# Kernel optimization log

Measured on AMD Instinct MI355X. Metric: run time of the kernel, lower is better.

## Reference

```python
import jax, jax.numpy as jnp
import numpy as np

Nx, Nu, Ny, Np, H = 2, 1, 2, 8, 32
Nz = Np * (Nx + Nu)  # 24
B, T = 4096, 256
F, V, Delta = 0.1, 1.0, 1.0  # ps.squeeze(), volume, sample time
ymean = jnp.array([0.5, 0.5], jnp.float32)
ystd = jnp.array([0.3, 0.2], jnp.float32)
umean = jnp.array([1.0], jnp.float32)
ustd = jnp.array([0.5], jnp.float32)


def fnn(x, params):
    # dense layers: tanh hidden, linear output
    for W, b in params[:-1]:
        x = jnp.tanh(x @ W + b)
    W, b = params[-1]
    return x @ W + b


def fxzu(x, z, u, p1, p2, p3):
    # dCa/dt = F*(Caf-Ca)/V - r1 ; dCb/dt = -F*Cb/V + r1 - 3*r2 + r3
    Castd, Cbstd = ystd[0:1], ystd[1:2]
    r1 = fnn(x[:, 0:1], p1) * Castd
    r2 = fnn(x[:, 1:2], p2) * Cbstd
    r3 = fnn(z, p3) * Cbstd
    xs = x * ystd + ymean
    us = u * ustd + umean
    Ca, Cb, Caf = xs[:, 0:1], xs[:, 1:2], us[:, 0:1]
    dCa = F * (Caf - Ca) / V - r1
    dCb = -F * Cb / V + r1 - 3.0 * r2 + r3
    return jnp.concatenate([dCa, dCb], axis=-1) / ystd


def interp(yseq):
    # (B,(Np+1)*Nx) -> (B, Np*Nx): midpoints of consecutive Nx-blocks
    b = yseq.shape[0]
    y = yseq.reshape(b, Np + 1, Nx)
    return (0.5 * (y[:, :-1] + y[:, 1:])).reshape(b, Np * Nx)


def run(useq, xz0, p1, p2, p3):
    def step(xz, u):
        x, z = xz[:, :Nx], xz[:, Nx:]
        xpseq, upseq = z[:, :Np * Nx], z[:, Np * Nx:]
        k1 = fxzu(x, z, u, p1, p2, p3)
        z23 = jnp.concatenate([interp(jnp.concatenate([xpseq, x], -1)), upseq], -1)
        k2 = fxzu(x + Delta * k1 / 2, z23, u, p1, p2, p3)
        k3 = fxzu(x + Delta * k2 / 2, z23, u, p1, p2, p3)
        z4 = jnp.concatenate([xpseq[:, Nx:], x, upseq], -1)
        k4 = fxzu(x + Delta * k3, z4, u, p1, p2, p3)
        xplus = x + (Delta / 6.0) * (k1 + 2 * k2 + 2 * k3 + k4)
        zplus = jnp.concatenate([xpseq[:, Nx:], x, upseq[:, Nu:], u], -1)
        return jnp.concatenate([xplus, zplus], -1), x  # output is pre-update x
    _, ys = jax.lax.scan(step, xz0, jnp.swapaxes(useq, 0, 1))
    return jnp.swapaxes(ys, 0, 1)  # (B, T, Ny)


def setup_inputs() -> dict:
    key = jax.random.key(0)
    ks = jax.random.split(key, 12)
    inp = {
        'useq': jax.random.normal(ks[0], (B, T, Nu), jnp.float32),
        'xz0': jax.random.normal(ks[1], (B, Nx + Nz), jnp.float32),
    }
    dims = {'r1': [1, H, H, 1], 'r2': [1, H, H, 1], 'r3': [Nz, H, H, 1]}
    i = 2
    for name, ds in dims.items():
        for l, (din, dout) in enumerate(zip(ds[:-1], ds[1:])):
            inp[f'{name}W{l}'] = jax.random.normal(ks[i], (din, dout), jnp.float32) / np.sqrt(din).astype(np.float32)
            inp[f'{name}b{l}'] = jnp.zeros((dout,), jnp.float32)
            i += 1
    return inp


def reference(useq, xz0, r1W0, r1b0, r1W1, r1b1, r1W2, r1b2,
              r2W0, r2b0, r2W1, r2b1, r2W2, r2b2,
              r3W0, r3b0, r3W1, r3b1, r3W2, r3b2):
    p1 = [(r1W0, r1b0), (r1W1, r1b1), (r1W2, r1b2)]
    p2 = [(r2W0, r2b0), (r2W1, r2b1), (r2W2, r2b2)]
    p3 = [(r3W0, r3b0), (r3W1, r3b1), (r3W2, r3b2)]
    return run(useq, xz0, p1, p2, p3)
```

## Files before the change

### kernel.cpp

```cpp
#include <hip/hip_runtime.h>

#define DEVINL static __device__ __forceinline__
#define CFENCE() asm volatile("" ::: "memory")

typedef float v2f __attribute__((ext_vector_type(2)));

DEVINL v2f mk2(float a, float b) { v2f r; r.x = a; r.y = b; return r; }
DEVINL v2f pkfma(v2f a, v2f b, v2f c) { return __builtin_elementwise_fma(a, b, c); }

constexpr float KE = 2.885390081777927f;

#if __has_builtin(__builtin_amdgcn_exp2f)
DEVINL float exp2_fast(float x) { return __builtin_amdgcn_exp2f(x); }
#else
DEVINL float exp2_fast(float x) { return __expf(x * 0.6931471805599453f); }
#endif

DEVINL float tanh_pre(float t) {
  float e = exp2_fast(t);
  return 1.0f - 2.0f * __builtin_amdgcn_rcpf(e + 1.0f);
}

template <int CTRL>
DEVINL float dpp_add(float v) {
  int t = __builtin_amdgcn_update_dpp(0, __float_as_int(v), CTRL, 0xF, 0xF, true);
  return v + __int_as_float(t);
}
DEVINL float rsum32(float v) {
  v = dpp_add<0xB1>(v);
  v = dpp_add<0x4E>(v);
  v = dpp_add<0x141>(v);
  v = dpp_add<0x140>(v);
  v += __int_as_float(__builtin_amdgcn_ds_swizzle(__float_as_int(v), 0x401F));
  return v;
}

DEVINL float dot32(const float* hrow, const v2f* W, float bias) {
  const float4* hp = (const float4*)hrow;
  v2f a0 = mk2(bias, 0.f), a1 = mk2(0.f, 0.f);
  v2f a2 = mk2(0.f, 0.f), a3 = mk2(0.f, 0.f);
#pragma unroll
  for (int q = 0; q < 8; q += 2) {
    float4 x = hp[q], y = hp[q + 1];
    a0 = pkfma(mk2(x.x, x.y), W[2 * q + 0], a0);
    a1 = pkfma(mk2(x.z, x.w), W[2 * q + 1], a1);
    a2 = pkfma(mk2(y.x, y.y), W[2 * q + 2], a2);
    a3 = pkfma(mk2(y.z, y.w), W[2 * q + 3], a3);
  }
  v2f s = (a0 + a1) + (a2 + a3);
  return s.x + s.y;
}
DEVINL float pdot16(const float* hrow, const v2f* W) {
  const float4* hp = (const float4*)hrow;
  v2f a0 = mk2(0.f, 0.f), a1 = mk2(0.f, 0.f);
  float4 x = hp[0], y = hp[1];
  a0 = pkfma(mk2(x.x, x.y), W[0], a0);
  a1 = pkfma(mk2(x.z, x.w), W[1], a1);
  a0 = pkfma(mk2(y.x, y.y), W[2], a0);
  a1 = pkfma(mk2(y.z, y.w), W[3], a1);
  x = hp[2]; y = hp[3];
  a0 = pkfma(mk2(x.x, x.y), W[4], a0);
  a1 = pkfma(mk2(x.z, x.w), W[5], a1);
  a0 = pkfma(mk2(y.x, y.y), W[6], a0);
  a1 = pkfma(mk2(y.z, y.w), W[7], a1);
  v2f s = a0 + a1;
  return s.x + s.y;
}

constexpr int TSTEPS = 256;

__global__ __attribute__((amdgpu_flat_work_group_size(64, 64)))
__attribute__((amdgpu_waves_per_eu(4, 4))) void reac_kernel(
    const float* __restrict__ useq,
    const float* __restrict__ xz0,
    const float* __restrict__ r1W0, const float* __restrict__ r1b0,
    const float* __restrict__ r1W1, const float* __restrict__ r1b1,
    const float* __restrict__ r1W2, const float* __restrict__ r1b2,
    const float* __restrict__ r2W0, const float* __restrict__ r2b0,
    const float* __restrict__ r2W1, const float* __restrict__ r2b1,
    const float* __restrict__ r2W2, const float* __restrict__ r2b2,
    const float* __restrict__ r3W0, const float* __restrict__ r3b0,
    const float* __restrict__ r3W1, const float* __restrict__ r3b1,
    const float* __restrict__ r3W2, const float* __restrict__ r3b2,
    float2* __restrict__ out)
{
  const int lane = threadIdx.x;
  const int j = lane & 31;
  const bool hi = lane >= 32;
  const int b = blockIdx.x;
  const int xaddr = ((lane ^ 32) << 2);

  auto xchg = [&](float v) -> float {
    return __int_as_float(__builtin_amdgcn_ds_bpermute(xaddr, __float_as_int(v)));
  };

  const float* W0p = hi ? r2W0 : r1W0;
  const float* B0p = hi ? r2b0 : r1b0;
  const float* W1p = hi ? r2W1 : r1W1;
  const float* B1p = hi ? r2b1 : r1b1;
  const float* W2p = hi ? r2W2 : r1W2;
  const float* B2p = hi ? r2b2 : r1b2;
  const float sc = hi ? 0.2f : 0.3f;
  float w0K = W0p[j] * KE, b0K = B0p[j] * KE;
  float b1K = B1p[j] * KE;
  float w2sc = W2p[j] * sc, b2sc = B2p[0] * sc;

  v2f W1v[16];
#pragma unroll
  for (int k = 0; k < 16; ++k)
    W1v[k] = mk2(W1p[(2 * k) * 32 + j] * KE, W1p[(2 * k + 1) * 32 + j] * KE);

  v2f W0Cv[12];
#pragma unroll
  for (int m = 0; m < 12; ++m)
    W0Cv[m] = mk2(r3W0[(2 * m) * 32 + j] * KE, r3W0[(2 * m + 1) * 32 + j] * KE);
  const int kbase = hi ? 16 : 0;
  v2f W1Cv[8];
#pragma unroll
  for (int k = 0; k < 8; ++k)
    W1Cv[k] = mk2(r3W1[(kbase + 2 * k) * 32 + j] * KE,
                  r3W1[(kbase + 2 * k + 1) * 32 + j] * KE);
  float b0CK = r3b0[j] * KE, b1CK = r3b1[j] * KE;
  float w2C02 = r3W2[j] * 0.2f;
  float b2Cs = r3b2[0] * 0.2f - 0.05f;

  __shared__ __align__(16) float zs[24];
  __shared__ __align__(16) float zb[16];
  __shared__ __align__(16) float h12[2][32];
  __shared__ __align__(16) float hR3[3][32];

  float x0 = xz0[b * 26 + 0];
  float x1 = xz0[b * 26 + 1];
  if (!hi && j < 24) zs[j] = xz0[b * 26 + 2 + j];
  CFENCE();

  auto stage = [&](float sxv, float syv, float rcp_, float CafF,
                   float& kx, float& ky) {
    float s = hi ? syv : sxv;
    float h = tanh_pre(fmaf(s, w0K, b0K));
    CFENCE();
    h12[hi][j] = h;
    CFENCE();
    float a = dot32(&h12[hi][0], W1v, b1K);
    float r = rsum32(tanh_pre(a) * w2sc) + b2sc;
    float rp = xchg(r);
    float ra = hi ? rp : r;
    float rb = hi ? r : rp;
    float dCa = fmaf(-0.03f, sxv, CafF) - ra;
    float dCb = fmaf(-0.02f, syv, fmaf(-3.0f, rb, ra) + rcp_);
    kx = dCa * (1.0f / 0.3f);
    ky = dCb * (1.0f / 0.2f);
  };

  float u = useq[b * TSTEPS];

  for (int t = 0; t < TSTEPS; ++t) {
    int tn = (t < TSTEPS - 1) ? (t + 1) : t;
    float u_nxt = useq[b * TSTEPS + tn];
    float CafF = fmaf(u, 0.05f, 0.05f);

    if (lane == 0) out[b * TSTEPS + t] = make_float2(x0, x1);

    CFENCE();
    if (!hi && j < 16) {
      zb[j] = (j < 14) ? zs[j + 2] : ((j == 14) ? x0 : x1);
    }
    CFENCE();

    const float4* zp = (const float4*)(hi ? &zb[0] : &zs[0]);
    float4 z0 = zp[0], z1 = zp[1], z2 = zp[2], z3 = zp[3];
    const float4* up = (const float4*)&zs[16];
    float4 u0 = up[0], u1 = up[1];
    v2f aa = mk2(b0CK, 0.f), ab = mk2(0.f, 0.f);
    aa = pkfma(mk2(z0.x, z0.y), W0Cv[0], aa);
    ab = pkfma(mk2(z0.z, z0.w), W0Cv[1], ab);
    aa = pkfma(mk2(z1.x, z1.y), W0Cv[2], aa);
    ab = pkfma(mk2(z1.z, z1.w), W0Cv[3], ab);
    aa = pkfma(mk2(z2.x, z2.y), W0Cv[4], aa);
    ab = pkfma(mk2(z2.z, z2.w), W0Cv[5], ab);
    aa = pkfma(mk2(z3.x, z3.y), W0Cv[6], aa);
    ab = pkfma(mk2(z3.z, z3.w), W0Cv[7], ab);
    aa = pkfma(mk2(u0.x, u0.y), W0Cv[8], aa);
    ab = pkfma(mk2(u0.z, u0.w), W0Cv[9], ab);
    aa = pkfma(mk2(u1.x, u1.y), W0Cv[10], aa);
    ab = pkfma(mk2(u1.z, u1.w), W0Cv[11], ab);
    v2f as = aa + ab;
    float A = as.x + as.y;
    float Ap = xchg(A);
    float tA = tanh_pre(A);
    if (!hi) {
      hR3[0][j] = tA;
      hR3[1][j] = tanh_pre(0.5f * (A + Ap));
    } else {
      hR3[2][j] = tA;
    }
    CFENCE();
    float p0 = pdot16(&hR3[0][kbase], W1Cv);
    float p1 = pdot16(&hR3[1][kbase], W1Cv);
    float p2 = pdot16(&hR3[2][kbase], W1Cv);
    float o0 = p0 + xchg(p0) + b1CK;
    float o1 = p1 + xchg(p1) + b1CK;
    float o2 = p2 + xchg(p2) + b1CK;
    float rc1  = rsum32(tanh_pre(o0) * w2C02) + b2Cs;
    float rc23 = rsum32(tanh_pre(o1) * w2C02) + b2Cs;
    float rc4  = rsum32(tanh_pre(o2) * w2C02) + b2Cs;

    float kx1, ky1, kx2, ky2, kx3, ky3, kx4, ky4;
    stage(x0, x1, rc1, CafF, kx1, ky1);
    stage(fmaf(kx1, 0.5f, x0), fmaf(ky1, 0.5f, x1), rc23, CafF, kx2, ky2);
    stage(fmaf(kx2, 0.5f, x0), fmaf(ky2, 0.5f, x1), rc23, CafF, kx3, ky3);
    stage(x0 + kx3, x1 + ky3, rc4, CafF, kx4, ky4);

    float znew = 0.0f;
    bool updz = (!hi) && (j < 24);
    if (updz) znew = (j < 16) ? zb[j] : ((j < 23) ? zs[j + 1] : u);
    CFENCE();
    if (updz) zs[j] = znew;
    x0 += (kx1 + 2.0f * (kx2 + kx3) + kx4) * (1.0f / 6.0f);
    x1 += (ky1 + 2.0f * (ky2 + ky3) + ky4) * (1.0f / 6.0f);
    u = u_nxt;
    CFENCE();
  }
}

extern "C" void kernel_launch(void* const* d_in, const int* in_sizes, int n_in,
                              void* d_out, int out_size, void* d_ws, size_t ws_size,
                              hipStream_t stream) {
  const float* p[20];
  for (int i = 0; i < 20; ++i) p[i] = (const float*)d_in[i];
  reac_kernel<<<dim3(4096), dim3(64), 0, stream>>>(
      p[0], p[1], p[2], p[3], p[4], p[5], p[6], p[7], p[8], p[9], p[10],
      p[11], p[12], p[13], p[14], p[15], p[16], p[17], p[18], p[19],
      (float2*)d_out);
}
```

Before: 871.6 us.

## Process two batch samples per wavefront to interleave independent dependency chains

Each 64-lane block now handles two batch elements instead of one, interleaving their RK4 stages so two independent latency chains (LDS round trips, DPP reductions, bpermutes) can overlap within a wave. The weight registers are shared across both samples. The grid is halved and waves_per_eu drops from 4 to 2, so occupancy falls and each thread has more live state. The gain depends on whether the added instruction-level parallelism outweighs the loss of wave-level parallelism.

```diff
diff --git a/kernel.cpp b/kernel.cpp
--- a/kernel.cpp
+++ b/kernel.cpp
@@ -70,7 +70,7 @@
 constexpr int TSTEPS = 256;
 
 __global__ __attribute__((amdgpu_flat_work_group_size(64, 64)))
-__attribute__((amdgpu_waves_per_eu(4, 4))) void reac_kernel(
+__attribute__((amdgpu_waves_per_eu(2, 2))) void reac_kernel(
     const float* __restrict__ useq,
     const float* __restrict__ xz0,
     const float* __restrict__ r1W0, const float* __restrict__ r1b0,
@@ -87,7 +87,7 @@
   const int lane = threadIdx.x;
   const int j = lane & 31;
   const bool hi = lane >= 32;
-  const int b = blockIdx.x;
+  const int b0 = blockIdx.x * 2;
   const int xaddr = ((lane ^ 32) << 2);
 
   auto xchg = [&](float v) -> float {
@@ -124,101 +124,160 @@
   float w2C02 = r3W2[j] * 0.2f;
   float b2Cs = r3b2[0] * 0.2f - 0.05f;
 
-  __shared__ __align__(16) float zs[24];
-  __shared__ __align__(16) float zb[16];
-  __shared__ __align__(16) float h12[2][32];
-  __shared__ __align__(16) float hR3[3][32];
-
-  float x0 = xz0[b * 26 + 0];
-  float x1 = xz0[b * 26 + 1];
-  if (!hi && j < 24) zs[j] = xz0[b * 26 + 2 + j];
+  __shared__ __align__(16) float zs[2][24];
+  __shared__ __align__(16) float zb[2][16];
+  __shared__ __align__(16) float h12[2][2][32];
+  __shared__ __align__(16) float hR3[2][3][32];
+
+  float x0[2], x1[2], u[2];
+#pragma unroll
+  for (int s = 0; s < 2; ++s) {
+    x0[s] = xz0[(b0 + s) * 26 + 0];
+    x1[s] = xz0[(b0 + s) * 26 + 1];
+    if (!hi && j < 24) zs[s][j] = xz0[(b0 + s) * 26 + 2 + j];
+    u[s] = useq[(b0 + s) * TSTEPS];
+  }
   CFENCE();
 
-  auto stage = [&](float sxv, float syv, float rcp_, float CafF,
-                   float& kx, float& ky) {
-    float s = hi ? syv : sxv;
-    float h = tanh_pre(fmaf(s, w0K, b0K));
-    CFENCE();
-    h12[hi][j] = h;
-    CFENCE();
-    float a = dot32(&h12[hi][0], W1v, b1K);
-    float r = rsum32(tanh_pre(a) * w2sc) + b2sc;
-    float rp = xchg(r);
-    float ra = hi ? rp : r;
-    float rb = hi ? r : rp;
-    float dCa = fmaf(-0.03f, sxv, CafF) - ra;
-    float dCb = fmaf(-0.02f, syv, fmaf(-3.0f, rb, ra) + rcp_);
-    kx = dCa * (1.0f / 0.3f);
-    ky = dCb * (1.0f / 0.2f);
+  auto stage2 = [&](const float* sxv, const float* syv, const float* rcp_,
+                    const float* CafF, float* kx, float* ky) {
+    CFENCE();
+#pragma unroll
+    for (int s = 0; s < 2; ++s) {
+      float sv = hi ? syv[s] : sxv[s];
+      h12[s][hi][j] = tanh_pre(fmaf(sv, w0K, b0K));
+    }
+    CFENCE();
+    float r[2];
+#pragma unroll
+    for (int s = 0; s < 2; ++s) {
+      float a = dot32(&h12[s][hi][0], W1v, b1K);
+      r[s] = rsum32(tanh_pre(a) * w2sc) + b2sc;
+    }
+#pragma unroll
+    for (int s = 0; s < 2; ++s) {
+      float rp = xchg(r[s]);
+      float ra = hi ? rp : r[s];
+      float rb = hi ? r[s] : rp;
+      float dCa = fmaf(-0.03f, sxv[s], CafF[s]) - ra;
+      float dCb = fmaf(-0.02f, syv[s], fmaf(-3.0f, rb, ra) + rcp_[s]);
+      kx[s] = dCa * (1.0f / 0.3f);
+      ky[s] = dCb * (1.0f / 0.2f);
+    }
   };
-
-  float u = useq[b * TSTEPS];
 
   for (int t = 0; t < TSTEPS; ++t) {
     int tn = (t < TSTEPS - 1) ? (t + 1) : t;
-    float u_nxt = useq[b * TSTEPS + tn];
-    float CafF = fmaf(u, 0.05f, 0.05f);
-
-    if (lane == 0) out[b * TSTEPS + t] = make_float2(x0, x1);
+    float u_nxt[2], CafF[2];
+#pragma unroll
+    for (int s = 0; s < 2; ++s) {
+      u_nxt[s] = useq[(b0 + s) * TSTEPS + tn];
+      CafF[s] = fmaf(u[s], 0.05f, 0.05f);
+    }
+
+    if (lane < 2) {
+      float a = lane ? x0[1] : x0[0];
+      float c = lane ? x1[1] : x1[0];
+      out[(b0 + lane) * TSTEPS + t] = make_float2(a, c);
+    }
 
     CFENCE();
     if (!hi && j < 16) {
-      zb[j] = (j < 14) ? zs[j + 2] : ((j == 14) ? x0 : x1);
-    }
-    CFENCE();
-
-    const float4* zp = (const float4*)(hi ? &zb[0] : &zs[0]);
-    float4 z0 = zp[0], z1 = zp[1], z2 = zp[2], z3 = zp[3];
-    const float4* up = (const float4*)&zs[16];
-    float4 u0 = up[0], u1 = up[1];
-    v2f aa = mk2(b0CK, 0.f), ab = mk2(0.f, 0.f);
-    aa = pkfma(mk2(z0.x, z0.y), W0Cv[0], aa);
-    ab = pkfma(mk2(z0.z, z0.w), W0Cv[1], ab);
-    aa = pkfma(mk2(z1.x, z1.y), W0Cv[2], aa);
-    ab = pkfma(mk2(z1.z, z1.w), W0Cv[3], ab);
-    aa = pkfma(mk2(z2.x, z2.y), W0Cv[4], aa);
-    ab = pkfma(mk2(z2.z, z2.w), W0Cv[5], ab);
-    aa = pkfma(mk2(z3.x, z3.y), W0Cv[6], aa);
-    ab = pkfma(mk2(z3.z, z3.w), W0Cv[7], ab);
-    aa = pkfma(mk2(u0.x, u0.y), W0Cv[8], aa);
-    ab = pkfma(mk2(u0.z, u0.w), W0Cv[9], ab);
-    aa = pkfma(mk2(u1.x, u1.y), W0Cv[10], aa);
-    ab = pkfma(mk2(u1.z, u1.w), W0Cv[11], ab);
-    v2f as = aa + ab;
-    float A = as.x + as.y;
-    float Ap = xchg(A);
-    float tA = tanh_pre(A);
-    if (!hi) {
-      hR3[0][j] = tA;
-      hR3[1][j] = tanh_pre(0.5f * (A + Ap));
-    } else {
-      hR3[2][j] = tA;
-    }
-    CFENCE();
-    float p0 = pdot16(&hR3[0][kbase], W1Cv);
-    float p1 = pdot16(&hR3[1][kbase], W1Cv);
-    float p2 = pdot16(&hR3[2][kbase], W1Cv);
-    float o0 = p0 + xchg(p0) + b1CK;
-    float o1 = p1 + xchg(p1) + b1CK;
-    float o2 = p2 + xchg(p2) + b1CK;
-    float rc1  = rsum32(tanh_pre(o0) * w2C02) + b2Cs;
-    float rc23 = rsum32(tanh_pre(o1) * w2C02) + b2Cs;
-    float rc4  = rsum32(tanh_pre(o2) * w2C02) + b2Cs;
-
-    float kx1, ky1, kx2, ky2, kx3, ky3, kx4, ky4;
-    stage(x0, x1, rc1, CafF, kx1, ky1);
-    stage(fmaf(kx1, 0.5f, x0), fmaf(ky1, 0.5f, x1), rc23, CafF, kx2, ky2);
-    stage(fmaf(kx2, 0.5f, x0), fmaf(ky2, 0.5f, x1), rc23, CafF, kx3, ky3);
-    stage(x0 + kx3, x1 + ky3, rc4, CafF, kx4, ky4);
-
-    float znew = 0.0f;
+#pragma unroll
+      for (int s = 0; s < 2; ++s)
+        zb[s][j] = (j < 14) ? zs[s][j + 2] : ((j == 14) ? x0[s] : x1[s]);
+    }
+    CFENCE();
+
+    float A[2];
+#pragma unroll
+    for (int s = 0; s < 2; ++s) {
+      const float4* zp = (const float4*)(hi ? &zb[s][0] : &zs[s][0]);
+      float4 z0 = zp[0], z1 = zp[1], z2 = zp[2], z3 = zp[3];
+      const float4* up = (const float4*)&zs[s][16];
+      float4 u0 = up[0], u1 = up[1];
+      v2f aa = mk2(b0CK, 0.f), ab = mk2(0.f, 0.f);
+      aa = pkfma(mk2(z0.x, z0.y), W0Cv[0], aa);
+      ab = pkfma(mk2(z0.z, z0.w), W0Cv[1], ab);
+      aa = pkfma(mk2(z1.x, z1.y), W0Cv[2], aa);
+      ab = pkfma(mk2(z1.z, z1.w), W0Cv[3], ab);
+      aa = pkfma(mk2(z2.x, z2.y), W0Cv[4], aa);
+      ab = pkfma(mk2(z2.z, z2.w), W0Cv[5], ab);
+      aa = pkfma(mk2(z3.x, z3.y), W0Cv[6], aa);
+      ab = pkfma(mk2(z3.z, z3.w), W0Cv[7], ab);
+      aa = pkfma(mk2(u0.x, u0.y), W0Cv[8], aa);
+      ab = pkfma(mk2(u0.z, u0.w), W0Cv[9], ab);
+      aa = pkfma(mk2(u1.x, u1.y), W0Cv[10], aa);
+      ab = pkfma(mk2(u1.z, u1.w), W0Cv[11], ab);
+      v2f as = aa + ab;
+      A[s] = as.x + as.y;
+    }
+#pragma unroll
+    for (int s = 0; s < 2; ++s) {
+      float Ap = xchg(A[s]);
+      float tA = tanh_pre(A[s]);
+      if (!hi) {
+        hR3[s][0][j] = tA;
+        hR3[s][1][j] = tanh_pre(0.5f * (A[s] + Ap));
+      } else {
+        hR3[s][2][j] = tA;
+      }
+    }
+    CFENCE();
+    float rc1[2], rc23[2], rc4[2];
+#pragma unroll
+    for (int s = 0; s < 2; ++s) {
+      float p0 = pdot16(&hR3[s][0][kbase], W1Cv);
+      float p1 = pdot16(&hR3[s][1][kbase], W1Cv);
+      float p2 = pdot16(&hR3[s][2][kbase], W1Cv);
+      float o0 = p0 + xchg(p0) + b1CK;
+      float o1 = p1 + xchg(p1) + b1CK;
+      float o2 = p2 + xchg(p2) + b1CK;
+      rc1[s]  = rsum32(tanh_pre(o0) * w2C02) + b2Cs;
+      rc23[s] = rsum32(tanh_pre(o1) * w2C02) + b2Cs;
+      rc4[s]  = rsum32(tanh_pre(o2) * w2C02) + b2Cs;
+    }
+
+    float kx1[2], ky1[2], kx2[2], ky2[2], kx3[2], ky3[2], kx4[2], ky4[2];
+    stage2(x0, x1, rc1, CafF, kx1, ky1);
+    float sx[2], sy[2];
+#pragma unroll
+    for (int s = 0; s < 2; ++s) {
+      sx[s] = fmaf(kx1[s], 0.5f, x0[s]);
+      sy[s] = fmaf(ky1[s], 0.5f, x1[s]);
+    }
+    stage2(sx, sy, rc23, CafF, kx2, ky2);
+#pragma unroll
+    for (int s = 0; s < 2; ++s) {
+      sx[s] = fmaf(kx2[s], 0.5f, x0[s]);
+      sy[s] = fmaf(ky2[s], 0.5f, x1[s]);
+    }
+    stage2(sx, sy, rc23, CafF, kx3, ky3);
+#pragma unroll
+    for (int s = 0; s < 2; ++s) {
+      sx[s] = x0[s] + kx3[s];
+      sy[s] = x1[s] + ky3[s];
+    }
+    stage2(sx, sy, rc4, CafF, kx4, ky4);
+
+    float znew[2];
     bool updz = (!hi) && (j < 24);
-    if (updz) znew = (j < 16) ? zb[j] : ((j < 23) ? zs[j + 1] : u);
-    CFENCE();
-    if (updz) zs[j] = znew;
-    x0 += (kx1 + 2.0f * (kx2 + kx3) + kx4) * (1.0f / 6.0f);
-    x1 += (ky1 + 2.0f * (ky2 + ky3) + ky4) * (1.0f / 6.0f);
-    u = u_nxt;
+    if (updz) {
+#pragma unroll
+      for (int s = 0; s < 2; ++s)
+        znew[s] = (j < 16) ? zb[s][j] : ((j < 23) ? zs[s][j + 1] : u[s]);
+    }
+    CFENCE();
+    if (updz) {
+#pragma unroll
+      for (int s = 0; s < 2; ++s) zs[s][j] = znew[s];
+    }
+#pragma unroll
+    for (int s = 0; s < 2; ++s) {
+      x0[s] += (kx1[s] + 2.0f * (kx2[s] + kx3[s]) + kx4[s]) * (1.0f / 6.0f);
+      x1[s] += (ky1[s] + 2.0f * (ky2[s] + ky3[s]) + ky4[s]) * (1.0f / 6.0f);
+      u[s] = u_nxt[s];
+    }
     CFENCE();
   }
 }
@@ -228,7 +287,7 @@
                               hipStream_t stream) {
   const float* p[20];
   for (int i = 0; i < 20; ++i) p[i] = (const float*)d_in[i];
-  reac_kernel<<<dim3(4096), dim3(64), 0, stream>>>(
+  reac_kernel<<<dim3(2048), dim3(64), 0, stream>>>(
       p[0], p[1], p[2], p[3], p[4], p[5], p[6], p[7], p[8], p[9], p[10],
       p[11], p[12], p[13], p[14], p[15], p[16], p[17], p[18], p[19],
       (float2*)d_out);
```

Measured after the change: 1.003 ms. +15.1%, slower.

## Keep z history in registers as ring buffer and use DPP/readlane reductions

Applied to the files above, without the earlier changes.

Replaces the LDS-resident z history (zs/zb shared arrays with per-step shift copies) with per-thread register ring buffers for past states and inputs. The time loop is unrolled by 8 so ring indices are compile-time constants. The cross-half reductions switch from ds_swizzle plus bpermute to a DPP row-broadcast followed by readlane, which yields both halves' results as uniform values. This removes LDS traffic and shift work from every step, at the cost of more VGPRs (24 scalar r3 weights plus 24 history floats) and a larger unrolled body, with the first-layer dot done as scalar FMAs instead of packed ones.

```diff
diff --git a/kernel.cpp b/kernel.cpp
--- a/kernel.cpp
+++ b/kernel.cpp
@@ -26,13 +26,20 @@
   int t = __builtin_amdgcn_update_dpp(0, __float_as_int(v), CTRL, 0xF, 0xF, true);
   return v + __int_as_float(t);
 }
-DEVINL float rsum32(float v) {
+DEVINL float rowsum16(float v) {
   v = dpp_add<0xB1>(v);
   v = dpp_add<0x4E>(v);
   v = dpp_add<0x141>(v);
   v = dpp_add<0x140>(v);
-  v += __int_as_float(__builtin_amdgcn_ds_swizzle(__float_as_int(v), 0x401F));
   return v;
+}
+DEVINL float halves_total(float v) {
+  v = rowsum16(v);
+  v = dpp_add<0x142>(v);
+  return v;
+}
+DEVINL float rlane(float v, int l) {
+  return __int_as_float(__builtin_amdgcn_readlane(__float_as_int(v), l));
 }
 
 DEVINL float dot32(const float* hrow, const v2f* W, float bias) {
@@ -66,8 +73,6 @@
   v2f s = a0 + a1;
   return s.x + s.y;
 }
-
-constexpr int TSTEPS = 256;
 
 __global__ __attribute__((amdgpu_flat_work_group_size(64, 64)))
 __attribute__((amdgpu_waves_per_eu(4, 4))) void reac_kernel(
@@ -99,21 +104,19 @@
   const float* W1p = hi ? r2W1 : r1W1;
   const float* B1p = hi ? r2b1 : r1b1;
   const float* W2p = hi ? r2W2 : r1W2;
-  const float* B2p = hi ? r2b2 : r1b2;
   const float sc = hi ? 0.2f : 0.3f;
   float w0K = W0p[j] * KE, b0K = B0p[j] * KE;
   float b1K = B1p[j] * KE;
-  float w2sc = W2p[j] * sc, b2sc = B2p[0] * sc;
+  float w2sc = W2p[j] * sc;
 
   v2f W1v[16];
 #pragma unroll
   for (int k = 0; k < 16; ++k)
     W1v[k] = mk2(W1p[(2 * k) * 32 + j] * KE, W1p[(2 * k + 1) * 32 + j] * KE);
 
-  v2f W0Cv[12];
-#pragma unroll
-  for (int m = 0; m < 12; ++m)
-    W0Cv[m] = mk2(r3W0[(2 * m) * 32 + j] * KE, r3W0[(2 * m + 1) * 32 + j] * KE);
+  float W0C[24];
+#pragma unroll
+  for (int m = 0; m < 24; ++m) W0C[m] = r3W0[m * 32 + j] * KE;
   const int kbase = hi ? 16 : 0;
   v2f W1Cv[8];
 #pragma unroll
@@ -122,104 +125,94 @@
                   r3W1[(kbase + 2 * k + 1) * 32 + j] * KE);
   float b0CK = r3b0[j] * KE, b1CK = r3b1[j] * KE;
   float w2C02 = r3W2[j] * 0.2f;
-  float b2Cs = r3b2[0] * 0.2f - 0.05f;
-
-  __shared__ __align__(16) float zs[24];
-  __shared__ __align__(16) float zb[16];
+
+  const float b2sA = r1b2[0] * 0.3f;
+  const float b2sB = r2b2[0] * 0.2f;
+  const float b2Cs = r3b2[0] * 0.2f - 0.05f;
+
   __shared__ __align__(16) float h12[2][32];
   __shared__ __align__(16) float hR3[3][32];
 
   float x0 = xz0[b * 26 + 0];
   float x1 = xz0[b * 26 + 1];
-  if (!hi && j < 24) zs[j] = xz0[b * 26 + 2 + j];
-  CFENCE();
-
-  auto stage = [&](float sxv, float syv, float rcp_, float CafF,
+  float xp[16], up[8];
+#pragma unroll
+  for (int i = 0; i < 16; ++i) xp[i] = xz0[b * 26 + 2 + i];
+#pragma unroll
+  for (int i = 0; i < 8; ++i) up[i] = xz0[b * 26 + 18 + i];
+
+  auto stage = [&](float sxv, float syv, float rc_m05, float CafF,
                    float& kx, float& ky) {
-    float s = hi ? syv : sxv;
-    float h = tanh_pre(fmaf(s, w0K, b0K));
+    float sv = hi ? syv : sxv;
+    float h = tanh_pre(fmaf(sv, w0K, b0K));
     CFENCE();
     h12[hi][j] = h;
     CFENCE();
     float a = dot32(&h12[hi][0], W1v, b1K);
-    float r = rsum32(tanh_pre(a) * w2sc) + b2sc;
-    float rp = xchg(r);
-    float ra = hi ? rp : r;
-    float rb = hi ? r : rp;
+    float v = halves_total(tanh_pre(a) * w2sc);
+    float ra = rlane(v, 31) + b2sA;
+    float rb = rlane(v, 63) + b2sB;
     float dCa = fmaf(-0.03f, sxv, CafF) - ra;
-    float dCb = fmaf(-0.02f, syv, fmaf(-3.0f, rb, ra) + rcp_);
+    float dCb = fmaf(-0.02f, syv, fmaf(-3.0f, rb, ra) + rc_m05);
     kx = dCa * (1.0f / 0.3f);
     ky = dCb * (1.0f / 0.2f);
   };
 
-  float u = useq[b * TSTEPS];
-
-  for (int t = 0; t < TSTEPS; ++t) {
-    int tn = (t < TSTEPS - 1) ? (t + 1) : t;
-    float u_nxt = useq[b * TSTEPS + tn];
-    float CafF = fmaf(u, 0.05f, 0.05f);
-
-    if (lane == 0) out[b * TSTEPS + t] = make_float2(x0, x1);
-
-    CFENCE();
-    if (!hi && j < 16) {
-      zb[j] = (j < 14) ? zs[j + 2] : ((j == 14) ? x0 : x1);
+  for (int tb = 0; tb < 32; ++tb) {
+#pragma unroll
+    for (int p = 0; p < 8; ++p) {
+      const int t = tb * 8 + p;
+      float u = useq[b * 256 + t];
+      float CafF = fmaf(u, 0.05f, 0.05f);
+
+      if (lane == 0) out[b * 256 + t] = make_float2(x0, x1);
+
+      float A = b0CK;
+#pragma unroll
+      for (int i = 0; i < 14; ++i) {
+        float m = hi ? xp[(2 * p + 2 + i) & 15] : xp[(2 * p + i) & 15];
+        A = fmaf(m, W0C[i], A);
+      }
+      {
+        float m = hi ? x0 : xp[(2 * p + 14) & 15];
+        A = fmaf(m, W0C[14], A);
+        m = hi ? x1 : xp[(2 * p + 15) & 15];
+        A = fmaf(m, W0C[15], A);
+      }
+#pragma unroll
+      for (int i = 0; i < 8; ++i) A = fmaf(up[(p + i) & 7], W0C[16 + i], A);
+
+      float Ap = xchg(A);
+      float tA = tanh_pre(A);
+      CFENCE();
+      hR3[hi ? 2 : 0][j] = tA;
+      if (!hi) hR3[1][j] = tanh_pre(0.5f * (A + Ap));
+      CFENCE();
+      float p0 = pdot16(&hR3[0][kbase], W1Cv);
+      float p1 = pdot16(&hR3[1][kbase], W1Cv);
+      float p2 = pdot16(&hR3[2][kbase], W1Cv);
+      float o0 = p0 + xchg(p0) + b1CK;
+      float o1 = p1 + xchg(p1) + b1CK;
+      float o2 = p2 + xchg(p2) + b1CK;
+      float v0 = halves_total(tanh_pre(o0) * w2C02);
+      float v1 = halves_total(tanh_pre(o1) * w2C02);
+      float v2 = halves_total(tanh_pre(o2) * w2C02);
+      float rc1  = rlane(v0, 31) + b2Cs;
+      float rc23 = rlane(v1, 31) + b2Cs;
+      float rc4  = rlane(v2, 31) + b2Cs;
+
+      float kx1, ky1, kx2, ky2, kx3, ky3, kx4, ky4;
+      stage(x0, x1, rc1, CafF, kx1, ky1);
+      stage(fmaf(kx1, 0.5f, x0), fmaf(ky1, 0.5f, x1), rc23, CafF, kx2, ky2);
+      stage(fmaf(kx2, 0.5f, x0), fmaf(ky2, 0.5f, x1), rc23, CafF, kx3, ky3);
+      stage(x0 + kx3, x1 + ky3, rc4, CafF, kx4, ky4);
+
+      xp[(2 * p) & 15] = x0;
+      xp[(2 * p + 1) & 15] = x1;
+      up[p & 7] = u;
+      x0 += (kx1 + 2.0f * (kx2 + kx3) + kx4) * (1.0f / 6.0f);
+      x1 += (ky1 + 2.0f * (ky2 + ky3) + ky4) * (1.0f / 6.0f);
     }
-    CFENCE();
-
-    const float4* zp = (const float4*)(hi ? &zb[0] : &zs[0]);
-    float4 z0 = zp[0], z1 = zp[1], z2 = zp[2], z3 = zp[3];
-    const float4* up = (const float4*)&zs[16];
-    float4 u0 = up[0], u1 = up[1];
-    v2f aa = mk2(b0CK, 0.f), ab = mk2(0.f, 0.f);
-    aa = pkfma(mk2(z0.x, z0.y), W0Cv[0], aa);
-    ab = pkfma(mk2(z0.z, z0.w), W0Cv[1], ab);
-    aa = pkfma(mk2(z1.x, z1.y), W0Cv[2], aa);
-    ab = pkfma(mk2(z1.z, z1.w), W0Cv[3], ab);
-    aa = pkfma(mk2(z2.x, z2.y), W0Cv[4], aa);
-    ab = pkfma(mk2(z2.z, z2.w), W0Cv[5], ab);
-    aa = pkfma(mk2(z3.x, z3.y), W0Cv[6], aa);
-    ab = pkfma(mk2(z3.z, z3.w), W0Cv[7], ab);
-    aa = pkfma(mk2(u0.x, u0.y), W0Cv[8], aa);
-    ab = pkfma(mk2(u0.z, u0.w), W0Cv[9], ab);
-    aa = pkfma(mk2(u1.x, u1.y), W0Cv[10], aa);
-    ab = pkfma(mk2(u1.z, u1.w), W0Cv[11], ab);
-    v2f as = aa + ab;
-    float A = as.x + as.y;
-    float Ap = xchg(A);
-    float tA = tanh_pre(A);
-    if (!hi) {
-      hR3[0][j] = tA;
-      hR3[1][j] = tanh_pre(0.5f * (A + Ap));
-    } else {
-      hR3[2][j] = tA;
-    }
-    CFENCE();
-    float p0 = pdot16(&hR3[0][kbase], W1Cv);
-    float p1 = pdot16(&hR3[1][kbase], W1Cv);
-    float p2 = pdot16(&hR3[2][kbase], W1Cv);
-    float o0 = p0 + xchg(p0) + b1CK;
-    float o1 = p1 + xchg(p1) + b1CK;
-    float o2 = p2 + xchg(p2) + b1CK;
-    float rc1  = rsum32(tanh_pre(o0) * w2C02) + b2Cs;
-    float rc23 = rsum32(tanh_pre(o1) * w2C02) + b2Cs;
-    float rc4  = rsum32(tanh_pre(o2) * w2C02) + b2Cs;
-
-    float kx1, ky1, kx2, ky2, kx3, ky3, kx4, ky4;
-    stage(x0, x1, rc1, CafF, kx1, ky1);
-    stage(fmaf(kx1, 0.5f, x0), fmaf(ky1, 0.5f, x1), rc23, CafF, kx2, ky2);
-    stage(fmaf(kx2, 0.5f, x0), fmaf(ky2, 0.5f, x1), rc23, CafF, kx3, ky3);
-    stage(x0 + kx3, x1 + ky3, rc4, CafF, kx4, ky4);
-
-    float znew = 0.0f;
-    bool updz = (!hi) && (j < 24);
-    if (updz) znew = (j < 16) ? zb[j] : ((j < 23) ? zs[j + 1] : u);
-    CFENCE();
-    if (updz) zs[j] = znew;
-    x0 += (kx1 + 2.0f * (kx2 + kx3) + kx4) * (1.0f / 6.0f);
-    x1 += (ky1 + 2.0f * (ky2 + ky3) + ky4) * (1.0f / 6.0f);
-    u = u_nxt;
-    CFENCE();
   }
 }
 
```

Measured after the change: 2.339 ms. 168% more time.
